# Kernel optimization log

Hardware: AMD Instinct MI355X
Metric: run time of the kernel (lower is better)

The kernel has to match this reference:

```python
import jax, jax.numpy as jnp
import numpy as np

N_USERS = 100000
N_ITEMS = 50000
N_NODES = N_USERS + N_ITEMS
DIM = 64
N_HOPS = 3
NNZ = 3200000
BATCH = 4096
K = 4
DECAY = 1e-4


def setup_inputs() -> dict:
    key = jax.random.key(0)
    ks = jax.random.split(key, 8)
    user_embed = jax.random.normal(ks[0], (N_USERS, DIM), dtype=jnp.float32) * 0.1
    item_embed = jax.random.normal(ks[1], (N_ITEMS, DIM), dtype=jnp.float32) * 0.1
    adj_rows = jax.random.randint(ks[2], (NNZ,), 0, N_NODES, dtype=jnp.int32)
    adj_cols = jax.random.randint(ks[3], (NNZ,), 0, N_NODES, dtype=jnp.int32)
    # normalized-adjacency-like small positive values
    adj_vals = jax.random.uniform(ks[4], (NNZ,), dtype=jnp.float32) * 0.05
    users = jax.random.randint(ks[5], (BATCH,), 0, N_USERS, dtype=jnp.int32)
    pos_items = jax.random.randint(ks[6], (BATCH,), 0, N_ITEMS, dtype=jnp.int32)
    neg_items = jax.random.randint(ks[7], (BATCH, K), 0, N_ITEMS, dtype=jnp.int32)
    return {"user_embed": user_embed, "item_embed": item_embed,
            "adj_vals": adj_vals, "adj_rows": adj_rows, "adj_cols": adj_cols,
            "users": users, "pos_items": pos_items, "neg_items": neg_items}


def _gcn(user_embed, item_embed, adj_vals, adj_rows, adj_cols):
    """LightGCN propagation: n_hops of SpMM, stack per-hop embeddings."""
    all_embed = jnp.concatenate([user_embed, item_embed], axis=0)  # [N, d]
    agg = all_embed
    embs = [all_embed]
    for _ in range(N_HOPS):
        msg = adj_vals[:, None] * agg[adj_cols]                    # [nnz, d]
        agg = jax.ops.segment_sum(msg, adj_rows, num_segments=N_NODES)
        embs.append(agg)
    embs = jnp.stack(embs, axis=1)                                 # [N, hops+1, d]
    return embs[:N_USERS], embs[N_USERS:]


def reference(user_embed, item_embed, adj_vals, adj_rows, adj_cols,
              users, pos_items, neg_items):
    user_gcn, item_gcn = _gcn(user_embed, item_embed, adj_vals, adj_rows, adj_cols)
    u_g = user_gcn[users]            # [B, hops+1, d]
    p_g = item_gcn[pos_items]        # [B, hops+1, d]
    n_g = item_gcn[neg_items]        # [B, K, hops+1, d]
    # pooling == 'mean' over hop axis
    u_e = u_g.mean(axis=1)
    pos_e = p_g.mean(axis=1)
    neg_e = n_g.mean(axis=2)         # [B, K, d]
    pos_scores = jnp.sum(u_e * pos_e, axis=-1)                     # [B]
    neg_scores = jnp.sum(u_e[:, None, :] * neg_e, axis=-1)         # [B, K]
    # BCE with logits: labels 1 for pos, 0 for neg
    pos_loss = jax.nn.softplus(-pos_scores)
    neg_loss = jax.nn.softplus(neg_scores).sum(axis=1)
    mf_loss = pos_loss + neg_loss
    regularize = (jnp.sum(u_g[:, 0, :] ** 2)
                  + jnp.sum(p_g[:, 0, :] ** 2)
                  + jnp.sum(n_g[:, :, 0, :] ** 2)) / 2.0
    emb_loss = DECAY * regularize / BATCH
    return mf_loss.mean() + emb_loss
```

## Files before the change

### kernel.cpp

```cpp
#include <hip/hip_runtime.h>
#include <hip/hip_bf16.h>
#include <math.h>

#define N_USERS 100000
#define N_ITEMS 50000
#define N_NODES 150000
#define DIM     64
#define N_HOPS  3
#define NNZ     3200000
#define BATCH   4096
#define KNEG    4
#define DECAY   1e-4f
#define BATCH_TOT (BATCH * (2 + KNEG))

#define NBUCK   586
#define NCHUNK  512
#define CHUNK   (NNZ / NCHUNK)
#define CAP     8192
#define BH_N    (NBUCK * NCHUNK)
#define S1_N    ((BH_N + 255) / 256)
#define S2_N    ((S1_N + 255) / 256)

typedef unsigned short ushort_t;
typedef unsigned int uint_t;
typedef unsigned long long u64_t;
typedef float v2f __attribute__((ext_vector_type(2)));

#if __has_builtin(__builtin_amdgcn_cvt_pk_f32_fp8) && __has_builtin(__builtin_amdgcn_cvt_pk_fp8_f32)
#define HAVE_FP8_CVT 1
#else
#define HAVE_FP8_CVT 0
#endif

#if !HAVE_FP8_CVT
__device__ __forceinline__ float dec1_(uint_t b) {
    uint_t s = b >> 7, e = (b >> 3) & 15, m = b & 7;
    float mag = e ? __uint_as_float(((e + 120u) << 23) | (m << 20))
                  : (float)m * 0.001953125f;
    return s ? -mag : mag;
}
__device__ __forceinline__ uint_t enc1_(float x) {
    float ax = fabsf(x);
    uint_t s = (__float_as_uint(x) >> 31) << 7;
    if (!(ax > 0.f)) return s;
    if (ax >= 448.f) return s | 0x7E;
    if (ax < 0.015625f) {
        int m = (int)rintf(ax * 512.0f);
        if (m >= 8) return s | 0x08;
        return s | (uint_t)m;
    }
    uint_t u = __float_as_uint(ax);
    u += 0x7FFFF + ((u >> 20) & 1);
    int e = (int)((u >> 23) & 0xFF) - 127 + 7;
    if (e >= 16) return s | 0x7E;
    if (e <= 0)  return s | 0x08;
    return s | ((uint_t)e << 3) | ((u >> 20) & 7);
}
#endif

__device__ __forceinline__ void dec4(uint_t u, float* f) {
#if HAVE_FP8_CVT
    v2f lo = __builtin_amdgcn_cvt_pk_f32_fp8(u, false);
    v2f hi = __builtin_amdgcn_cvt_pk_f32_fp8(u, true);
    f[0] = lo[0]; f[1] = lo[1]; f[2] = hi[0]; f[3] = hi[1];
#else
    f[0] = dec1_(u & 255); f[1] = dec1_((u >> 8) & 255);
    f[2] = dec1_((u >> 16) & 255); f[3] = dec1_(u >> 24);
#endif
}

__device__ __forceinline__ uint_t enc4(const float* f) {
#if HAVE_FP8_CVT
    int t = __builtin_amdgcn_cvt_pk_fp8_f32(f[0], f[1], 0, false);
    t = __builtin_amdgcn_cvt_pk_fp8_f32(f[2], f[3], t, true);
    return (uint_t)t;
#else
    return enc1_(f[0]) | (enc1_(f[1]) << 8) | (enc1_(f[2]) << 16) | (enc1_(f[3]) << 24);
#endif
}


__global__ void k_bhist(const int* __restrict__ rows, int* __restrict__ bh) {
    __shared__ int hist[NBUCK];
    int t = threadIdx.x, b = blockIdx.x;
    for (int i = t; i < NBUCK; i += 256) hist[i] = 0;
    __syncthreads();
    int base = b * CHUNK;
    for (int e = base + t; e < base + CHUNK; e += 256)
        atomicAdd(&hist[rows[e] >> 8], 1);
    __syncthreads();
    for (int i = t; i < NBUCK; i += 256)
        bh[(size_t)i * NCHUNK + b] = hist[i];
}

__global__ void k_scanA(int* __restrict__ data, int* __restrict__ bsums, int n) {
    __shared__ int lds[256];
    int t = threadIdx.x;
    int i = blockIdx.x * 256 + t;
    int v = (i < n) ? data[i] : 0;
    lds[t] = v; __syncthreads();
    for (int o = 1; o < 256; o <<= 1) {
        int x = (t >= o) ? lds[t - o] : 0;
        __syncthreads();
        lds[t] += x;
        __syncthreads();
    }
    if (i < n) data[i] = lds[t] - v;
    if (t == 255) bsums[blockIdx.x] = lds[t];
}

__global__ void k_scan_small(int* __restrict__ data, int n) {
    __shared__ int lds[1024];
    int t = threadIdx.x;
    int v = (t < n) ? data[t] : 0;
    lds[t] = v; __syncthreads();
    for (int o = 1; o < 1024; o <<= 1) {
        int x = (t >= o) ? lds[t - o] : 0;
        __syncthreads();
        lds[t] += x;
        __syncthreads();
    }
    if (t < n) data[t] = lds[t] - v;
}

__global__ void k_addback(int* __restrict__ data, const int* __restrict__ offs, int n) {
    int i = blockIdx.x * blockDim.x + threadIdx.x;
    if (i < n) data[i] += offs[i >> 8];
}

__global__ __launch_bounds__(512) void k_scatter(
        const int* __restrict__ rows, const int* __restrict__ cols,
        const float* __restrict__ vals, const int* __restrict__ bh,
        u64_t* __restrict__ ebuf) {
    __shared__ u64_t stage[CHUNK];
    __shared__ int sexcl[NBUCK + 1];
    __shared__ int gbase[NBUCK];
    __shared__ int cursor[NBUCK];
    __shared__ int part[512];
    int t = threadIdx.x, b = blockIdx.x;
    for (int i = t; i < NBUCK; i += 512) {
        cursor[i] = 0;
        gbase[i] = bh[(size_t)i * NCHUNK + b];
    }
    __syncthreads();
    int base0 = b * CHUNK;
    for (int e = base0 + t; e < base0 + CHUNK; e += 512)
        atomicAdd(&cursor[rows[e] >> 8], 1);
    __syncthreads();
    int a0 = (2 * t     < NBUCK) ? cursor[2 * t]     : 0;
    int a1 = (2 * t + 1 < NBUCK) ? cursor[2 * t + 1] : 0;
    part[t] = a0 + a1;
    __syncthreads();
    for (int o = 1; o < 512; o <<= 1) {
        int x = (t >= o) ? part[t - o] : 0;
        __syncthreads();
        part[t] += x;
        __syncthreads();
    }
    int ebase = part[t] - (a0 + a1);
    if (2 * t < NBUCK)     sexcl[2 * t] = ebase;
    if (2 * t + 1 < NBUCK) sexcl[2 * t + 1] = ebase + a0;
    if (t == 0) sexcl[NBUCK] = CHUNK;
    __syncthreads();
    for (int i = t; i < NBUCK; i += 512) cursor[i] = sexcl[i];
    __syncthreads();
    for (int e = base0 + t; e < base0 + CHUNK; e += 512) {
        int r = rows[e];
        int slot = atomicAdd(&cursor[r >> 8], 1);
        stage[slot] = ((u64_t)(uint_t)__float_as_int(vals[e]) << 32)
                    | ((u64_t)(r & 255) << 18) | (u64_t)cols[e];
    }
    __syncthreads();
    int wid = t >> 6, lane = t & 63;
    for (int k = wid; k < NBUCK; k += 8) {
        int S = sexcl[k], E = sexcl[k + 1], G = gbase[k];
        for (int j = S + lane; j < E; j += 64)
            ebuf[G + j - S] = stage[j];
    }
}

__global__ void k_bucket_csr(const u64_t* __restrict__ ebuf, const int* __restrict__ bh,
                             int2* __restrict__ edges, int* __restrict__ row_ptr) {
    __shared__ u64_t stage[CAP];
    __shared__ int hist[256];
    __shared__ int sbuf[256];
    int t = threadIdx.x, b = blockIdx.x;
    int S = bh[(size_t)b * NCHUNK];
    int E = (b + 1 < NBUCK) ? bh[(size_t)(b + 1) * NCHUNK] : NNZ;
    int cnt = E - S;
    if (cnt > CAP) cnt = CAP;
    hist[t] = 0;
    __syncthreads();
    for (int i = t; i < cnt; i += 256) {
        u64_t v = ebuf[S + i];
        stage[i] = v;
        atomicAdd(&hist[(int)((v >> 18) & 255)], 1);
    }
    __syncthreads();
    int v = hist[t];
    sbuf[t] = v; __syncthreads();
    for (int o = 1; o < 256; o <<= 1) {
        int x = (t >= o) ? sbuf[t - o] : 0;
        __syncthreads();
        sbuf[t] += x;
        __syncthreads();
    }
    int excl = sbuf[t] - v;
    int grow = (b << 8) + t;
    if (grow < N_NODES) row_ptr[grow] = S + excl;
    if (b == 0 && t == 0) row_ptr[N_NODES] = NNZ;
    hist[t] = excl;
    __syncthreads();
    for (int i = t; i < cnt; i += 256) {
        u64_t pk = stage[i];
        int rl = (int)((pk >> 18) & 255);
        int slot = atomicAdd(&hist[rl], 1);
        edges[S + slot] = make_int2((int)(pk & 0x3FFFF), (int)(pk >> 32));
    }
}


__global__ void k_tofp8(const float* __restrict__ ue, const float* __restrict__ ie,
                        uint2* __restrict__ outq) {
    int idx = blockIdx.x * blockDim.x + threadIdx.x;
    const int total8 = N_NODES * DIM / 8;
    if (idx >= total8) return;
    const int u8 = N_USERS * DIM / 8;
    const float4* src = (idx < u8) ? (const float4*)ue + 2 * (size_t)idx
                                   : (const float4*)ie + 2 * (size_t)(idx - u8);
    float4 a = src[0], b = src[1];
    float fa[4] = {a.x, a.y, a.z, a.w};
    float fb[4] = {b.x, b.y, b.z, b.w};
    outq[idx] = make_uint2(enc4(fa), enc4(fb));
}

__device__ __forceinline__ void fma8(uint2 r, float v, float* acc) {
    float f[4];
    dec4(r.x, f);
    acc[0] += v * f[0]; acc[1] += v * f[1]; acc[2] += v * f[2]; acc[3] += v * f[3];
    dec4(r.y, f);
    acc[4] += v * f[0]; acc[5] += v * f[1]; acc[6] += v * f[2]; acc[7] += v * f[3];
}

__device__ __forceinline__ void row_accum8(const uint2* __restrict__ srcq,
                                           const int2* __restrict__ edges,
                                           int s, int e, int oct, int ol,
                                           float* acc) {
    int i = s;
    for (; i + 16 <= e; i += 16) {
        int2 e0 = edges[i + oct];
        int2 e1 = edges[i + 8 + oct];
        uint2 r0 = srcq[(size_t)e0.x * 8 + ol];
        uint2 r1 = srcq[(size_t)e1.x * 8 + ol];
        fma8(r0, __int_as_float(e0.y), acc);
        fma8(r1, __int_as_float(e1.y), acc);
    }
    for (; i + 8 <= e; i += 8) {
        int2 ed = edges[i + oct];
        uint2 r = srcq[(size_t)ed.x * 8 + ol];
        fma8(r, __int_as_float(ed.y), acc);
    }
    int rem = e - i;
    if (oct < rem) {
        int2 ed = edges[i + oct];
        uint2 r = srcq[(size_t)ed.x * 8 + ol];
        fma8(r, __int_as_float(ed.y), acc);
    }
}

__device__ __forceinline__ void oct_reduce(float* acc) {
    #pragma unroll
    for (int j = 0; j < 8; ++j) {
        acc[j] += __shfl_xor(acc[j], 8);
        acc[j] += __shfl_xor(acc[j], 16);
        acc[j] += __shfl_xor(acc[j], 32);
    }
}

__global__ void k_spmm(const uint2* __restrict__ srcq, uint2* __restrict__ outq,
                       const int* __restrict__ row_ptr, const int2* __restrict__ edges) {
    int w = (blockIdx.x * blockDim.x + threadIdx.x) >> 6;
    int lane = threadIdx.x & 63;
    if (w >= N_NODES) return;
    int oct = lane >> 3, ol = lane & 7;
    int s = row_ptr[w], e = row_ptr[w + 1];
    float acc[8] = {0.f, 0.f, 0.f, 0.f, 0.f, 0.f, 0.f, 0.f};
    row_accum8(srcq, edges, s, e, oct, ol, acc);
    oct_reduce(acc);
    if (oct == 0)
        outq[(size_t)w * 8 + ol] = make_uint2(enc4(acc), enc4(acc + 4));
}

__device__ __forceinline__ void batch_map(int w, const int* __restrict__ users,
                                          const int* __restrict__ pos, const int* __restrict__ neg,
                                          float* u_acc, float* p_acc, float* n_acc,
                                          int& node, float*& dst) {
    if (w < BATCH)            { node = users[w];                        dst = u_acc + (size_t)w * DIM; }
    else if (w < 2 * BATCH)   { int j = w - BATCH;     node = N_USERS + pos[j]; dst = p_acc + (size_t)j * DIM; }
    else                      { int j = w - 2 * BATCH; node = N_USERS + neg[j]; dst = n_acc + (size_t)j * DIM; }
}

__global__ void k_gather_init(const float* __restrict__ ue, const float* __restrict__ ie,
                              const int* __restrict__ users, const int* __restrict__ pos,
                              const int* __restrict__ neg,
                              float* __restrict__ u_acc, float* __restrict__ p_acc,
                              float* __restrict__ n_acc) {
    int w = (blockIdx.x * blockDim.x + threadIdx.x) >> 6;
    int lane = threadIdx.x & 63;
    if (w >= BATCH_TOT) return;
    int node; float* dst;
    batch_map(w, users, pos, neg, u_acc, p_acc, n_acc, node, dst);
    const float* srow = (node < N_USERS) ? ue + (size_t)node * DIM
                                         : ie + (size_t)(node - N_USERS) * DIM;
    dst[lane] = srow[lane];
}

__global__ void k_gather_accum(const uint_t* __restrict__ src,
                               const int* __restrict__ users, const int* __restrict__ pos,
                               const int* __restrict__ neg,
                               float* __restrict__ u_acc, float* __restrict__ p_acc,
                               float* __restrict__ n_acc) {
    int gid = blockIdx.x * blockDim.x + threadIdx.x;
    int w4 = gid >> 6;
    int lane = threadIdx.x & 63;
    int slot = w4 * 4 + (lane >> 4);
    int dquad = lane & 15;
    if (slot >= BATCH_TOT) return;
    int node; float* dst;
    batch_map(slot, users, pos, neg, u_acc, p_acc, n_acc, node, dst);
    float f[4];
    dec4(src[(size_t)node * 16 + dquad], f);
    float4* d4 = (float4*)(dst + 4 * dquad);
    float4 cur = *d4;
    cur.x += f[0]; cur.y += f[1]; cur.z += f[2]; cur.w += f[3];
    *d4 = cur;
}

__global__ void k_spmm_batch(const uint2* __restrict__ srcq,
                             const int* __restrict__ row_ptr, const int2* __restrict__ edges,
                             const int* __restrict__ users, const int* __restrict__ pos,
                             const int* __restrict__ neg,
                             float* __restrict__ u_acc, float* __restrict__ p_acc,
                             float* __restrict__ n_acc) {
    int w = (blockIdx.x * blockDim.x + threadIdx.x) >> 6;
    int lane = threadIdx.x & 63;
    if (w >= BATCH_TOT) return;
    int oct = lane >> 3, ol = lane & 7;
    int node; float* dst;
    batch_map(w, users, pos, neg, u_acc, p_acc, n_acc, node, dst);
    int s = row_ptr[node], e = row_ptr[node + 1];
    float acc[8] = {0.f, 0.f, 0.f, 0.f, 0.f, 0.f, 0.f, 0.f};
    row_accum8(srcq, edges, s, e, oct, ol, acc);
    oct_reduce(acc);
    if (oct == 0) {
        #pragma unroll
        for (int j = 0; j < 8; ++j) dst[8 * ol + j] += acc[j];
    }
}

__global__ void k_zero_out(float* out) { out[0] = 0.f; }

__device__ __forceinline__ float softplus(float x) {
    return log1pf(expf(-fabsf(x))) + fmaxf(x, 0.f);
}

__device__ __forceinline__ float wave_sum(float v) {
    for (int o = 32; o > 0; o >>= 1) v += __shfl_xor(v, o);
    return v;
}

__global__ void k_loss(const float* __restrict__ u_acc, const float* __restrict__ p_acc,
                       const float* __restrict__ n_acc,
                       const float* __restrict__ ue, const float* __restrict__ ie,
                       const int* __restrict__ users, const int* __restrict__ pos,
                       const int* __restrict__ neg, float* __restrict__ out) {
    int w = (blockIdx.x * blockDim.x + threadIdx.x) >> 6;
    int lane = threadIdx.x & 63;
    if (w >= BATCH) return;
    const float inv = 1.0f / (N_HOPS + 1);
    float u = u_acc[(size_t)w * DIM + lane] * inv;
    float p = p_acc[(size_t)w * DIM + lane] * inv;
    float pos_score = wave_sum(u * p);
    float loss = softplus(-pos_score);
    #pragma unroll
    for (int k = 0; k < KNEG; ++k) {
        float nk = n_acc[((size_t)w * KNEG + k) * DIM + lane] * inv;
        float neg_score = wave_sum(u * nk);
        loss += softplus(neg_score);
    }
    float u0 = ue[(size_t)users[w] * DIM + lane];
    float p0 = ie[(size_t)pos[w]  * DIM + lane];
    float r = u0 * u0 + p0 * p0;
    #pragma unroll
    for (int k = 0; k < KNEG; ++k) {
        float n0 = ie[(size_t)neg[w * KNEG + k] * DIM + lane];
        r += n0 * n0;
    }
    r = wave_sum(r);
    float contrib = loss * (1.0f / BATCH) + (DECAY * 0.5f / BATCH) * r;
    if (lane == 0) atomicAdd(out, contrib);
}


extern "C" void kernel_launch(void* const* d_in, const int* in_sizes, int n_in,
                              void* d_out, int out_size, void* d_ws, size_t ws_size,
                              hipStream_t stream) {
    const float* user_embed = (const float*)d_in[0];
    const float* item_embed = (const float*)d_in[1];
    const float* adj_vals   = (const float*)d_in[2];
    const int*   adj_rows   = (const int*)d_in[3];
    const int*   adj_cols   = (const int*)d_in[4];
    const int*   users      = (const int*)d_in[5];
    const int*   pos_items  = (const int*)d_in[6];
    const int*   neg_items  = (const int*)d_in[7];
    float* out = (float*)d_out;

    int2* edges   = (int2*)d_ws;
    u64_t* ebuf   = (u64_t*)(edges + NNZ);
    float* u_acc  = (float*)(ebuf + NNZ);
    float* p_acc  = u_acc + (size_t)BATCH * DIM;
    float* n_acc  = p_acc + (size_t)BATCH * DIM;
    uint2* bufB   = (uint2*)(n_acc + (size_t)BATCH * KNEG * DIM);
    uint2* buf1   = bufB + (size_t)N_NODES * 8;
    int* row_ptr  = (int*)(buf1 + (size_t)N_NODES * 8);
    int* bh       = row_ptr + N_NODES + 1;
    int* S1       = bh + BH_N;
    int* S2       = S1 + S1_N;
    uint2* buf0   = (uint2*)ebuf;

    const int T = 256;

    k_bhist<<<NCHUNK, 256, 0, stream>>>(adj_rows, bh);
    k_scanA<<<S1_N, 256, 0, stream>>>(bh, S1, BH_N);
    k_scanA<<<S2_N, 256, 0, stream>>>(S1, S2, S1_N);
    k_scan_small<<<1, 1024, 0, stream>>>(S2, S2_N);
    k_addback<<<(S1_N + T - 1) / T, T, 0, stream>>>(S1, S2, S1_N);
    k_addback<<<(BH_N + T - 1) / T, T, 0, stream>>>(bh, S1, BH_N);
    k_scatter<<<NCHUNK, 512, 0, stream>>>(adj_rows, adj_cols, adj_vals, bh, ebuf);
    k_bucket_csr<<<NBUCK, 256, 0, stream>>>(ebuf, bh, edges, row_ptr);

    k_tofp8<<<(N_NODES * DIM / 8 + T - 1) / T, T, 0, stream>>>(user_embed, item_embed, bufB);

    int gb = (BATCH_TOT * 64 + T - 1) / T;
    k_gather_init<<<gb, T, 0, stream>>>(user_embed, item_embed,
                                        users, pos_items, neg_items,
                                        u_acc, p_acc, n_acc);

    int sb = (N_NODES * 64 + T - 1) / T;
    int gb4 = ((BATCH_TOT / 4) * 64 + T - 1) / T;

    k_spmm<<<sb, T, 0, stream>>>(bufB, buf0, row_ptr, edges);
    k_gather_accum<<<gb4, T, 0, stream>>>((const uint_t*)buf0, users, pos_items, neg_items,
                                          u_acc, p_acc, n_acc);
    k_spmm<<<sb, T, 0, stream>>>(buf0, buf1, row_ptr, edges);
    k_gather_accum<<<gb4, T, 0, stream>>>((const uint_t*)buf1, users, pos_items, neg_items,
                                          u_acc, p_acc, n_acc);
    k_spmm_batch<<<gb, T, 0, stream>>>(buf1, row_ptr, edges,
                                       users, pos_items, neg_items,
                                       u_acc, p_acc, n_acc);

    k_zero_out<<<1, 1, 0, stream>>>(out);
    k_loss<<<(BATCH * 64 + T - 1) / T, T, 0, stream>>>(
        u_acc, p_acc, n_acc, user_embed, item_embed, users, pos_items, neg_items, out);
}
```

Measured before the change: 301.4 us.

## Fuse histogram into scatter pass and gather buckets from per-chunk sorted segments

The bucket histogram and the local sort into LDS now happen in one pass, so edges are read once before the global scan. Sorted chunks are written back contiguously, and the per-chunk bucket offsets are saved so that bucket_csr can pull each bucket's segments from every chunk. This removes one full read of rows. The separate gather_init kernel is also dropped: the first gather now overwrites instead of accumulating, and the loss kernel adds the hop-0 fp32 embeddings itself. In exchange, bucket_csr does many small, scattered segment reads, which may coalesce poorly.

```diff
diff --git a/kernel.cpp b/kernel.cpp
--- a/kernel.cpp
+++ b/kernel.cpp
@@ -80,17 +80,52 @@
 }
 
 
-__global__ void k_bhist(const int* __restrict__ rows, int* __restrict__ bh) {
+__global__ __launch_bounds__(512) void k_scatter(
+        const int* __restrict__ rows, const int* __restrict__ cols,
+        const float* __restrict__ vals, int* __restrict__ bh,
+        int* __restrict__ sloc, u64_t* __restrict__ ebuf) {
+    __shared__ u64_t stage[CHUNK];
     __shared__ int hist[NBUCK];
+    __shared__ int cursor[NBUCK];
+    __shared__ int part[512];
     int t = threadIdx.x, b = blockIdx.x;
-    for (int i = t; i < NBUCK; i += 256) hist[i] = 0;
-    __syncthreads();
-    int base = b * CHUNK;
-    for (int e = base + t; e < base + CHUNK; e += 256)
+    for (int i = t; i < NBUCK; i += 512) hist[i] = 0;
+    __syncthreads();
+    int base0 = b * CHUNK;
+    for (int e = base0 + t; e < base0 + CHUNK; e += 512)
         atomicAdd(&hist[rows[e] >> 8], 1);
     __syncthreads();
-    for (int i = t; i < NBUCK; i += 256)
+    for (int i = t; i < NBUCK; i += 512)
         bh[(size_t)i * NCHUNK + b] = hist[i];
+    int a0 = (2 * t     < NBUCK) ? hist[2 * t]     : 0;
+    int a1 = (2 * t + 1 < NBUCK) ? hist[2 * t + 1] : 0;
+    part[t] = a0 + a1;
+    __syncthreads();
+    for (int o = 1; o < 512; o <<= 1) {
+        int x = (t >= o) ? part[t - o] : 0;
+        __syncthreads();
+        part[t] += x;
+        __syncthreads();
+    }
+    int ebase = part[t] - (a0 + a1);
+    __syncthreads();
+    if (2 * t < NBUCK)     hist[2 * t] = ebase;
+    if (2 * t + 1 < NBUCK) hist[2 * t + 1] = ebase + a0;
+    __syncthreads();
+    for (int i = t; i < NBUCK; i += 512) {
+        sloc[(size_t)b * NBUCK + i] = hist[i];
+        cursor[i] = hist[i];
+    }
+    __syncthreads();
+    for (int e = base0 + t; e < base0 + CHUNK; e += 512) {
+        int r = rows[e];
+        int slot = atomicAdd(&cursor[r >> 8], 1);
+        stage[slot] = ((u64_t)(uint_t)__float_as_int(vals[e]) << 32)
+                    | ((u64_t)(r & 255) << 18) | (u64_t)cols[e];
+    }
+    __syncthreads();
+    for (int i = t; i < CHUNK; i += 512)
+        ebuf[base0 + i] = stage[i];
 }
 
 __global__ void k_scanA(int* __restrict__ data, int* __restrict__ bsums, int n) {
@@ -128,58 +163,8 @@
     if (i < n) data[i] += offs[i >> 8];
 }
 
-__global__ __launch_bounds__(512) void k_scatter(
-        const int* __restrict__ rows, const int* __restrict__ cols,
-        const float* __restrict__ vals, const int* __restrict__ bh,
-        u64_t* __restrict__ ebuf) {
-    __shared__ u64_t stage[CHUNK];
-    __shared__ int sexcl[NBUCK + 1];
-    __shared__ int gbase[NBUCK];
-    __shared__ int cursor[NBUCK];
-    __shared__ int part[512];
-    int t = threadIdx.x, b = blockIdx.x;
-    for (int i = t; i < NBUCK; i += 512) {
-        cursor[i] = 0;
-        gbase[i] = bh[(size_t)i * NCHUNK + b];
-    }
-    __syncthreads();
-    int base0 = b * CHUNK;
-    for (int e = base0 + t; e < base0 + CHUNK; e += 512)
-        atomicAdd(&cursor[rows[e] >> 8], 1);
-    __syncthreads();
-    int a0 = (2 * t     < NBUCK) ? cursor[2 * t]     : 0;
-    int a1 = (2 * t + 1 < NBUCK) ? cursor[2 * t + 1] : 0;
-    part[t] = a0 + a1;
-    __syncthreads();
-    for (int o = 1; o < 512; o <<= 1) {
-        int x = (t >= o) ? part[t - o] : 0;
-        __syncthreads();
-        part[t] += x;
-        __syncthreads();
-    }
-    int ebase = part[t] - (a0 + a1);
-    if (2 * t < NBUCK)     sexcl[2 * t] = ebase;
-    if (2 * t + 1 < NBUCK) sexcl[2 * t + 1] = ebase + a0;
-    if (t == 0) sexcl[NBUCK] = CHUNK;
-    __syncthreads();
-    for (int i = t; i < NBUCK; i += 512) cursor[i] = sexcl[i];
-    __syncthreads();
-    for (int e = base0 + t; e < base0 + CHUNK; e += 512) {
-        int r = rows[e];
-        int slot = atomicAdd(&cursor[r >> 8], 1);
-        stage[slot] = ((u64_t)(uint_t)__float_as_int(vals[e]) << 32)
-                    | ((u64_t)(r & 255) << 18) | (u64_t)cols[e];
-    }
-    __syncthreads();
-    int wid = t >> 6, lane = t & 63;
-    for (int k = wid; k < NBUCK; k += 8) {
-        int S = sexcl[k], E = sexcl[k + 1], G = gbase[k];
-        for (int j = S + lane; j < E; j += 64)
-            ebuf[G + j - S] = stage[j];
-    }
-}
-
 __global__ void k_bucket_csr(const u64_t* __restrict__ ebuf, const int* __restrict__ bh,
+                             const int* __restrict__ sloc,
                              int2* __restrict__ edges, int* __restrict__ row_ptr) {
     __shared__ u64_t stage[CAP];
     __shared__ int hist[256];
@@ -191,11 +176,21 @@
     if (cnt > CAP) cnt = CAP;
     hist[t] = 0;
     __syncthreads();
-    for (int i = t; i < cnt; i += 256) {
-        u64_t v = ebuf[S + i];
-        stage[i] = v;
-        atomicAdd(&hist[(int)((v >> 18) & 255)], 1);
-    }
+    int wid = t >> 6, lane = t & 63;
+    int sub = lane >> 3, j0 = lane & 7;
+    for (int c = wid * 8; c < NCHUNK; c += 32) {
+        int bch = c + sub;
+        int lo = sloc[(size_t)bch * NBUCK + b];
+        int hi = (b + 1 < NBUCK) ? sloc[(size_t)bch * NBUCK + b + 1] : CHUNK;
+        int dst = bh[(size_t)b * NCHUNK + bch] - S;
+        for (int j = j0; j < hi - lo; j += 8) {
+            if (dst + j < CAP)
+                stage[dst + j] = ebuf[(size_t)bch * CHUNK + lo + j];
+        }
+    }
+    __syncthreads();
+    for (int i = t; i < cnt; i += 256)
+        atomicAdd(&hist[(int)((stage[i] >> 18) & 255)], 1);
     __syncthreads();
     int v = hist[t];
     sbuf[t] = v; __syncthreads();
@@ -300,21 +295,7 @@
     else                      { int j = w - 2 * BATCH; node = N_USERS + neg[j]; dst = n_acc + (size_t)j * DIM; }
 }
 
-__global__ void k_gather_init(const float* __restrict__ ue, const float* __restrict__ ie,
-                              const int* __restrict__ users, const int* __restrict__ pos,
-                              const int* __restrict__ neg,
-                              float* __restrict__ u_acc, float* __restrict__ p_acc,
-                              float* __restrict__ n_acc) {
-    int w = (blockIdx.x * blockDim.x + threadIdx.x) >> 6;
-    int lane = threadIdx.x & 63;
-    if (w >= BATCH_TOT) return;
-    int node; float* dst;
-    batch_map(w, users, pos, neg, u_acc, p_acc, n_acc, node, dst);
-    const float* srow = (node < N_USERS) ? ue + (size_t)node * DIM
-                                         : ie + (size_t)(node - N_USERS) * DIM;
-    dst[lane] = srow[lane];
-}
-
+template<int INIT>
 __global__ void k_gather_accum(const uint_t* __restrict__ src,
                                const int* __restrict__ users, const int* __restrict__ pos,
                                const int* __restrict__ neg,
@@ -331,9 +312,13 @@
     float f[4];
     dec4(src[(size_t)node * 16 + dquad], f);
     float4* d4 = (float4*)(dst + 4 * dquad);
-    float4 cur = *d4;
-    cur.x += f[0]; cur.y += f[1]; cur.z += f[2]; cur.w += f[3];
-    *d4 = cur;
+    if (INIT) {
+        *d4 = make_float4(f[0], f[1], f[2], f[3]);
+    } else {
+        float4 cur = *d4;
+        cur.x += f[0]; cur.y += f[1]; cur.z += f[2]; cur.w += f[3];
+        *d4 = cur;
+    }
 }
 
 __global__ void k_spmm_batch(const uint2* __restrict__ srcq,
@@ -378,22 +363,19 @@
     int lane = threadIdx.x & 63;
     if (w >= BATCH) return;
     const float inv = 1.0f / (N_HOPS + 1);
-    float u = u_acc[(size_t)w * DIM + lane] * inv;
-    float p = p_acc[(size_t)w * DIM + lane] * inv;
+    float u0 = ue[(size_t)users[w] * DIM + lane];
+    float p0 = ie[(size_t)pos[w]  * DIM + lane];
+    float u = (u_acc[(size_t)w * DIM + lane] + u0) * inv;
+    float p = (p_acc[(size_t)w * DIM + lane] + p0) * inv;
     float pos_score = wave_sum(u * p);
     float loss = softplus(-pos_score);
-    #pragma unroll
-    for (int k = 0; k < KNEG; ++k) {
-        float nk = n_acc[((size_t)w * KNEG + k) * DIM + lane] * inv;
-        float neg_score = wave_sum(u * nk);
-        loss += softplus(neg_score);
-    }
-    float u0 = ue[(size_t)users[w] * DIM + lane];
-    float p0 = ie[(size_t)pos[w]  * DIM + lane];
     float r = u0 * u0 + p0 * p0;
     #pragma unroll
     for (int k = 0; k < KNEG; ++k) {
         float n0 = ie[(size_t)neg[w * KNEG + k] * DIM + lane];
+        float nk = (n_acc[((size_t)w * KNEG + k) * DIM + lane] + n0) * inv;
+        float neg_score = wave_sum(u * nk);
+        loss += softplus(neg_score);
         r += n0 * n0;
     }
     r = wave_sum(r);
@@ -426,35 +408,31 @@
     int* bh       = row_ptr + N_NODES + 1;
     int* S1       = bh + BH_N;
     int* S2       = S1 + S1_N;
+    int* sloc     = S2 + S2_N + 11;
     uint2* buf0   = (uint2*)ebuf;
 
     const int T = 256;
 
-    k_bhist<<<NCHUNK, 256, 0, stream>>>(adj_rows, bh);
+    k_scatter<<<NCHUNK, 512, 0, stream>>>(adj_rows, adj_cols, adj_vals, bh, sloc, ebuf);
     k_scanA<<<S1_N, 256, 0, stream>>>(bh, S1, BH_N);
     k_scanA<<<S2_N, 256, 0, stream>>>(S1, S2, S1_N);
     k_scan_small<<<1, 1024, 0, stream>>>(S2, S2_N);
     k_addback<<<(S1_N + T - 1) / T, T, 0, stream>>>(S1, S2, S1_N);
     k_addback<<<(BH_N + T - 1) / T, T, 0, stream>>>(bh, S1, BH_N);
-    k_scatter<<<NCHUNK, 512, 0, stream>>>(adj_rows, adj_cols, adj_vals, bh, ebuf);
-    k_bucket_csr<<<NBUCK, 256, 0, stream>>>(ebuf, bh, edges, row_ptr);
+    k_bucket_csr<<<NBUCK, 256, 0, stream>>>(ebuf, bh, sloc, edges, row_ptr);
 
     k_tofp8<<<(N_NODES * DIM / 8 + T - 1) / T, T, 0, stream>>>(user_embed, item_embed, bufB);
 
+    int sb = (N_NODES * 64 + T - 1) / T;
     int gb = (BATCH_TOT * 64 + T - 1) / T;
-    k_gather_init<<<gb, T, 0, stream>>>(user_embed, item_embed,
-                                        users, pos_items, neg_items,
-                                        u_acc, p_acc, n_acc);
-
-    int sb = (N_NODES * 64 + T - 1) / T;
     int gb4 = ((BATCH_TOT / 4) * 64 + T - 1) / T;
 
     k_spmm<<<sb, T, 0, stream>>>(bufB, buf0, row_ptr, edges);
-    k_gather_accum<<<gb4, T, 0, stream>>>((const uint_t*)buf0, users, pos_items, neg_items,
-                                          u_acc, p_acc, n_acc);
+    k_gather_accum<1><<<gb4, T, 0, stream>>>((const uint_t*)buf0, users, pos_items, neg_items,
+                                             u_acc, p_acc, n_acc);
     k_spmm<<<sb, T, 0, stream>>>(buf0, buf1, row_ptr, edges);
-    k_gather_accum<<<gb4, T, 0, stream>>>((const uint_t*)buf1, users, pos_items, neg_items,
-                                          u_acc, p_acc, n_acc);
+    k_gather_accum<0><<<gb4, T, 0, stream>>>((const uint_t*)buf1, users, pos_items, neg_items,
+                                             u_acc, p_acc, n_acc);
     k_spmm_batch<<<gb, T, 0, stream>>>(buf1, row_ptr, edges,
                                        users, pos_items, neg_items,
                                        u_acc, p_acc, n_acc);
```

New measurement: 307.0 us. No clear change (+1.9%).
